# Performance work log

Measured on AMD Instinct MI355X. Metric: run time of the kernel, lower is better.

Reference implementation:

```python
import jax, jax.numpy as jnp
import numpy as np

H, W, N = 1024, 2048, 1572864
NF, NP, NIN = 32, 3, 5


def _linear_init(key, fan_in, fan_out):
    kw, kb = jax.random.split(key)
    bound = 1.0 / np.sqrt(fan_in)
    w = jax.random.uniform(kw, (fan_in, fan_out), jnp.float32, -bound, bound)
    b = jax.random.uniform(kb, (fan_out,), jnp.float32, -bound, bound)
    return w, b


def setup_inputs() -> dict:
    key = jax.random.key(0)
    ks = jax.random.split(key, 8)
    # grid: sub-pixel source coordinates, (2, N), x-row then y-row
    gx = jax.random.uniform(ks[0], (1, N), jnp.float32) * (W - 1)
    gy = jax.random.uniform(ks[1], (1, N), jnp.float32) * (H - 1)
    grid = jnp.concatenate([gx, gy], axis=0)
    # yi: unique flat pixel indices (torch index-assign assumes no duplicates)
    yi = jax.random.permutation(ks[2], H * W)[:N].astype(jnp.int32)
    # m: near-identity homography so the projective denominator stays well-conditioned
    m = jnp.eye(3, dtype=jnp.float32) + 0.05 * jax.random.normal(ks[3], (3, 3), jnp.float32)
    W1, b1 = _linear_init(ks[4], NIN, NF)
    W2, b2 = _linear_init(ks[5], NF, NF)
    W3, b3 = _linear_init(ks[6], NF, NF)
    W4, b4 = _linear_init(ks[7], NF, NP)
    return {"grid": grid, "yi": yi, "m": m,
            "W1": W1, "b1": b1, "W2": W2, "b2": b2,
            "W3": W3, "b3": b3, "W4": W4, "b4": b4,
            "size_h": H, "size_w": W}


def _calc_dsda_projective(m, h, w):
    # Area scale (Jacobian determinant magnitude) of the homography m at each
    # output pixel: |det(m)| / |m20*x + m21*y + m22|^3, flattened row-major (H*W,)
    xs = jnp.arange(w, dtype=jnp.float32)
    ys = jnp.arange(h, dtype=jnp.float32)
    denom = m[2, 0] * xs[None, :] + m[2, 1] * ys[:, None] + m[2, 2]  # (H, W)
    det = jnp.linalg.det(m)
    return (jnp.abs(det) / (jnp.abs(denom) ** 3)).reshape(-1)


def reference(grid, yi, m, W1, b1, W2, b2, W3, b3, W4, b4, size_h, size_w):
    h, w = size_h, size_w
    # --- feature construction (torch.no_grad block) ---
    dsda = _calc_dsda_projective(m, h, w)[yi][:, None]          # (N, 1) gather
    g = grid.T                                                  # (N, 2)
    gf = jnp.floor(g)
    tl = g - gf                                                 # x-fx, y-fy
    br = 1.0 - tl                                               # fx+1-x, fy+1-y
    x = jax.lax.stop_gradient(jnp.concatenate([tl, br, dsda], axis=1))  # (N, 5)
    # --- tiny 4-layer MLP ---
    hdd = jax.nn.relu(x @ W1 + b1)
    hdd = jax.nn.relu(hdd @ W2 + b2)
    hdd = jax.nn.relu(hdd @ W3 + b3)
    logits = hdd @ W4 + b4                                      # (N, NP)
    wgt = jax.nn.softmax(logits, axis=1)
    # --- scatter back to spatial layout ---
    w_spatial = jnp.zeros((h * w, NP), dtype=wgt.dtype).at[yi].set(wgt)
    return w_spatial.reshape(1, 1, h, w, NP)
```

## Files before the change

kernel.cpp:

```cpp
#include <hip/hip_runtime.h>


#define W_IMG 2048
#define NF    32
#define PST   80
#define BUF   (64 * PST)

typedef __attribute__((ext_vector_type(8))) _Float16 f16x8;
typedef __attribute__((ext_vector_type(4))) _Float16 f16x4;
typedef __attribute__((ext_vector_type(4))) float    f32x4;

__global__ __launch_bounds__(256) void fill_zero(float* __restrict__ out, int n) {
    int n4 = n >> 2;
    float4* o4 = (float4*)out;
    int stride = gridDim.x * blockDim.x;
    for (int i = blockIdx.x * blockDim.x + threadIdx.x; i < n4; i += stride)
        o4[i] = make_float4(0.f, 0.f, 0.f, 0.f);
    int t = (n4 << 2) + (blockIdx.x * blockDim.x + threadIdx.x);
    if (t < n) out[t] = 0.f;
}

__global__ __launch_bounds__(256, 4) void msampler_mlp(
    const float* __restrict__ grid,
    const int*   __restrict__ yi,
    const float* __restrict__ m,
    const float* __restrict__ W1, const float* __restrict__ b1,
    const float* __restrict__ W2, const float* __restrict__ b2,
    const float* __restrict__ W3, const float* __restrict__ b3,
    const float* __restrict__ W4, const float* __restrict__ b4,
    float* __restrict__ out, int N)
{
    const int tid  = threadIdx.x;
    const int lane = tid & 63;
    const int wave = tid >> 6;
    const int lm   = lane & 15;
    const int lq   = lane >> 4;
    const int i    = blockIdx.x * 256 + tid;
    const int ic   = i < N ? i : N - 1;

    __shared__ __align__(16) char smem[4 * 2 * BUF];
    char* bufA = smem + wave * (2 * BUF);
    char* bufB = bufA + BUF;

    f16x8 a1[2], a2[2], a3[2];
    f32x4 cb1[2], cb2[2], cb3[2];
#pragma unroll
    for (int mh = 0; mh < 2; ++mh) {
        int outc = 16 * mh + lm;
#pragma unroll
        for (int j = 0; j < 8; ++j) {
            int k = lq * 8 + j;
            a1[mh][j] = (k < 5) ? (_Float16)W1[k * NF + outc] : (_Float16)0.0f;
            a2[mh][j] = (_Float16)W2[k * NF + outc];
            a3[mh][j] = (_Float16)W3[k * NF + outc];
        }
#pragma unroll
        for (int r = 0; r < 4; ++r) {
            int o = 16 * mh + lq * 4 + r;
            cb1[mh][r] = b1[o];
            cb2[mh][r] = b2[o];
            cb3[mh][r] = b3[o];
        }
    }

    float gx = grid[ic];
    float gy = grid[N + ic];
    int   y  = yi[ic];
    int   py = y >> 11;
    int   px = y & (W_IMG - 1);

    float m00=m[0], m01=m[1], m02=m[2];
    float m10=m[3], m11=m[4], m12=m[5];
    float m20=m[6], m21=m[7], m22=m[8];
    float det = m00*(m11*m22 - m12*m21)
              - m01*(m10*m22 - m12*m20)
              + m02*(m10*m21 - m11*m20);
    float denom = m20*(float)px + m21*(float)py + m22;
    float ad    = fabsf(denom);
    float dsda  = fabsf(det) / (ad*ad*ad);
    dsda = fminf(dsda, 60000.f);

    float fx = gx - floorf(gx);
    float fy = gy - floorf(gy);

    {
        f16x8 f0;
        f0[0] = (_Float16)fx;        f0[1] = (_Float16)fy;
        f0[2] = (_Float16)(1.f-fx);  f0[3] = (_Float16)(1.f-fy);
        f0[4] = (_Float16)dsda;      f0[5] = (_Float16)0.0f;
        f0[6] = (_Float16)0.0f;      f0[7] = (_Float16)0.0f;
        f16x8 z = f0 - f0;
        char* row = bufA + lane * PST;
        *(f16x8*)(row)      = f0;
        *(f16x8*)(row + 16) = z;
        *(f16x8*)(row + 32) = z;
        *(f16x8*)(row + 48) = z;
    }
    __syncthreads();

#define MFMA_LAYER(SRC, DST, AF, CB)                                          \
    {                                                                         \
        f16x8 bf[4];                                                          \
        _Pragma("unroll")                                                     \
        for (int g = 0; g < 4; ++g)                                           \
            bf[g] = *(const f16x8*)((SRC) + (16*g + lm) * PST + lq * 16);     \
        _Pragma("unroll")                                                     \
        for (int mh = 0; mh < 2; ++mh) {                                      \
            _Pragma("unroll")                                                 \
            for (int g = 0; g < 4; ++g) {                                     \
                f32x4 d = __builtin_amdgcn_mfma_f32_16x16x32_f16(             \
                    AF[mh], bf[g], CB[mh], 0, 0, 0);                          \
                f16x4 o;                                                      \
                _Pragma("unroll")                                             \
                for (int r = 0; r < 4; ++r)                                   \
                    o[r] = (_Float16)fminf(fmaxf(d[r], 0.f), 60000.f);        \
                *(f16x4*)((DST) + (16*g + lm) * PST + (16*mh + lq*4) * 2) = o;\
            }                                                                 \
        }                                                                     \
    }

    MFMA_LAYER(bufA, bufB, a1, cb1)
    __syncthreads();
    MFMA_LAYER(bufB, bufA, a2, cb2)
    __syncthreads();
    MFMA_LAYER(bufA, bufB, a3, cb3)
    __syncthreads();
#undef MFMA_LAYER

    float l0 = b4[0], l1 = b4[1], l2 = b4[2];
    {
        const char* row = bufB + lane * PST;
#pragma unroll
        for (int c = 0; c < 4; ++c) {
            f16x8 hv = *(const f16x8*)(row + c * 16);
#pragma unroll
            for (int j = 0; j < 8; ++j) {
                float h = (float)hv[j];
                int k = c * 8 + j;
                l0 = fmaf(h, W4[k*3 + 0], l0);
                l1 = fmaf(h, W4[k*3 + 1], l1);
                l2 = fmaf(h, W4[k*3 + 2], l2);
            }
        }
    }
    float mx = fmaxf(l0, fmaxf(l1, l2));
    float e0 = __expf(l0 - mx), e1 = __expf(l1 - mx), e2 = __expf(l2 - mx);
    float inv = 1.f / (e0 + e1 + e2);

    if (i < N) {
        int o = y * 3;
        out[o + 0] = e0 * inv;
        out[o + 1] = e1 * inv;
        out[o + 2] = e2 * inv;
    }
}

extern "C" void kernel_launch(void* const* d_in, const int* in_sizes, int n_in,
                              void* d_out, int out_size, void* d_ws, size_t ws_size,
                              hipStream_t stream) {
    const float* grid = (const float*)d_in[0];
    const int*   yi   = (const int*)  d_in[1];
    const float* m    = (const float*)d_in[2];
    const float* W1   = (const float*)d_in[3];
    const float* b1   = (const float*)d_in[4];
    const float* W2   = (const float*)d_in[5];
    const float* b2   = (const float*)d_in[6];
    const float* W3   = (const float*)d_in[7];
    const float* b3   = (const float*)d_in[8];
    const float* W4   = (const float*)d_in[9];
    const float* b4   = (const float*)d_in[10];
    float* out = (float*)d_out;

    int N = in_sizes[1];

    fill_zero<<<1024, 256, 0, stream>>>(out, out_size);

    int block = 256;
    int grid_sz = (N + block - 1) / block;
    msampler_mlp<<<grid_sz, block, 0, stream>>>(
        grid, yi, m, W1, b1, W2, b2, W3, b3, W4, b4, out, N);
}
```

Before: 130.5 us.

## Process two tiles per wave with in-place MFMA buffer and MFMA final layer

```diff
diff --git a/kernel.cpp b/kernel.cpp
--- a/kernel.cpp
+++ b/kernel.cpp
@@ -3,8 +3,6 @@
 
 #define W_IMG 2048
 #define NF    32
-#define PST   80
-#define BUF   (64 * PST)
 
 typedef __attribute__((ext_vector_type(8))) _Float16 f16x8;
 typedef __attribute__((ext_vector_type(4))) _Float16 f16x4;
@@ -35,15 +33,12 @@
     const int wave = tid >> 6;
     const int lm   = lane & 15;
     const int lq   = lane >> 4;
-    const int i    = blockIdx.x * 256 + tid;
-    const int ic   = i < N ? i : N - 1;
-
-    __shared__ __align__(16) char smem[4 * 2 * BUF];
-    char* bufA = smem + wave * (2 * BUF);
-    char* bufB = bufA + BUF;
-
-    f16x8 a1[2], a2[2], a3[2];
-    f32x4 cb1[2], cb2[2], cb3[2];
+
+    __shared__ __align__(16) char smem[4 * 8192];
+    char* buf = smem + wave * 8192;
+
+    f16x8 a1[2], a2[2], a3[2], a4;
+    f32x4 cb1[2], cb2[2], cb3[2], cb4;
 #pragma unroll
     for (int mh = 0; mh < 2; ++mh) {
         int outc = 16 * mh + lm;
@@ -62,12 +57,16 @@
             cb3[mh][r] = b3[o];
         }
     }
-
-    float gx = grid[ic];
-    float gy = grid[N + ic];
-    int   y  = yi[ic];
-    int   py = y >> 11;
-    int   px = y & (W_IMG - 1);
+#pragma unroll
+    for (int j = 0; j < 8; ++j) {
+        int k = lq * 8 + j;
+        a4[j] = (lm < 3) ? (_Float16)W4[k * 3 + lm] : (_Float16)0.0f;
+    }
+#pragma unroll
+    for (int r = 0; r < 4; ++r) {
+        int o = lq * 4 + r;
+        cb4[r] = (o < 3) ? b4[o] : 0.f;
+    }
 
     float m00=m[0], m01=m[1], m02=m[2];
     float m10=m[3], m11=m[4], m12=m[5];
@@ -75,83 +74,103 @@
     float det = m00*(m11*m22 - m12*m21)
               - m01*(m10*m22 - m12*m20)
               + m02*(m10*m21 - m11*m20);
-    float denom = m20*(float)px + m21*(float)py + m22;
-    float ad    = fabsf(denom);
-    float dsda  = fabsf(det) / (ad*ad*ad);
-    dsda = fminf(dsda, 60000.f);
-
-    float fx = gx - floorf(gx);
-    float fy = gy - floorf(gy);
-
+    float adet = fabsf(det);
+
+    const int i0 = blockIdx.x * 512 + wave * 128;
+    int ya[2];
+#pragma unroll
+    for (int t = 0; t < 2; ++t) {
+        int i  = i0 + t * 64 + lane;
+        int ic = i < N ? i : N - 1;
+        float gx = grid[ic];
+        float gy = grid[N + ic];
+        int   y  = yi[ic];
+        ya[t] = y;
+        int py = y >> 11;
+        int px = y & (W_IMG - 1);
+        float denom = m20*(float)px + m21*(float)py + m22;
+        float ad    = fabsf(denom);
+        float dsda  = fminf(adet / (ad*ad*ad), 60000.f);
+        float fx = gx - floorf(gx);
+        float fy = gy - floorf(gy);
+        f16x8 f;
+        f[0] = (_Float16)fx;         f[1] = (_Float16)fy;
+        f[2] = (_Float16)(1.f-fx);   f[3] = (_Float16)(1.f-fy);
+        f[4] = (_Float16)dsda;       f[5] = (_Float16)0.0f;
+        f[6] = (_Float16)0.0f;       f[7] = (_Float16)0.0f;
+        int g = t * 4 + lq;
+        *(f16x8*)(buf + g * 1024 + lm * 16) = f;
+    }
     {
-        f16x8 f0;
-        f0[0] = (_Float16)fx;        f0[1] = (_Float16)fy;
-        f0[2] = (_Float16)(1.f-fx);  f0[3] = (_Float16)(1.f-fy);
-        f0[4] = (_Float16)dsda;      f0[5] = (_Float16)0.0f;
-        f0[6] = (_Float16)0.0f;      f0[7] = (_Float16)0.0f;
-        f16x8 z = f0 - f0;
-        char* row = bufA + lane * PST;
-        *(f16x8*)(row)      = f0;
-        *(f16x8*)(row + 16) = z;
-        *(f16x8*)(row + 32) = z;
-        *(f16x8*)(row + 48) = z;
-    }
-    __syncthreads();
-
-#define MFMA_LAYER(SRC, DST, AF, CB)                                          \
-    {                                                                         \
-        f16x8 bf[4];                                                          \
-        _Pragma("unroll")                                                     \
-        for (int g = 0; g < 4; ++g)                                           \
-            bf[g] = *(const f16x8*)((SRC) + (16*g + lm) * PST + lq * 16);     \
-        _Pragma("unroll")                                                     \
-        for (int mh = 0; mh < 2; ++mh) {                                      \
-            _Pragma("unroll")                                                 \
-            for (int g = 0; g < 4; ++g) {                                     \
-                f32x4 d = __builtin_amdgcn_mfma_f32_16x16x32_f16(             \
-                    AF[mh], bf[g], CB[mh], 0, 0, 0);                          \
-                f16x4 o;                                                      \
-                _Pragma("unroll")                                             \
-                for (int r = 0; r < 4; ++r)                                   \
-                    o[r] = (_Float16)fminf(fmaxf(d[r], 0.f), 60000.f);        \
-                *(f16x4*)((DST) + (16*g + lm) * PST + (16*mh + lq*4) * 2) = o;\
-            }                                                                 \
-        }                                                                     \
-    }
-
-    MFMA_LAYER(bufA, bufB, a1, cb1)
-    __syncthreads();
-    MFMA_LAYER(bufB, bufA, a2, cb2)
-    __syncthreads();
-    MFMA_LAYER(bufA, bufB, a3, cb3)
-    __syncthreads();
-#undef MFMA_LAYER
-
-    float l0 = b4[0], l1 = b4[1], l2 = b4[2];
-    {
-        const char* row = bufB + lane * PST;
-#pragma unroll
-        for (int c = 0; c < 4; ++c) {
-            f16x8 hv = *(const f16x8*)(row + c * 16);
-#pragma unroll
-            for (int j = 0; j < 8; ++j) {
-                float h = (float)hv[j];
-                int k = c * 8 + j;
-                l0 = fmaf(h, W4[k*3 + 0], l0);
-                l1 = fmaf(h, W4[k*3 + 1], l1);
-                l2 = fmaf(h, W4[k*3 + 2], l2);
-            }
-        }
-    }
-    float mx = fmaxf(l0, fmaxf(l1, l2));
-    float e0 = __expf(l0 - mx), e1 = __expf(l1 - mx), e2 = __expf(l2 - mx);
-    float inv = 1.f / (e0 + e1 + e2);
-
-    if (i < N) {
-        int o = y * 3;
-        out[o + 0] = e0 * inv;
-        out[o + 1] = e1 * inv;
-        out[o + 2] = e2 * inv;
+        f16x8 z = {};
+#pragma unroll
+        for (int j = 0; j < 6; ++j) {
+            int T  = lane >> 3;
+            int ch = (lane & 7) + 8 * j;
+            *(f16x8*)(buf + T * 1024 + 256 + ch * 16) = z;
+        }
+    }
+
+    const int woff = ((lq >> 1) * 16 + lm) * 16 + (lq & 1) * 8;
+
+#define LAYER(AF, CB)                                                          \
+    _Pragma("unroll")                                                          \
+    for (int tg = 0; tg < 2; ++tg) {                                           \
+        f16x8 bf[4];                                                           \
+        _Pragma("unroll")                                                      \
+        for (int q = 0; q < 4; ++q)                                            \
+            bf[q] = *(const f16x8*)(buf + (tg*4 + q) * 1024 + lane * 16);      \
+        _Pragma("unroll")                                                      \
+        for (int q = 0; q < 4; ++q) {                                          \
+            int T = tg * 4 + q;                                                \
+            _Pragma("unroll")                                                  \
+            for (int mh = 0; mh < 2; ++mh) {                                   \
+                f32x4 d = __builtin_amdgcn_mfma_f32_16x16x32_f16(              \
+                    AF[mh], bf[q], CB[mh], 0, 0, 0);                           \
+                f16x4 o;                                                       \
+                _Pragma("unroll")                                              \
+                for (int r = 0; r < 4; ++r)                                    \
+                    o[r] = (_Float16)fminf(fmaxf(d[r], 0.f), 60000.f);         \
+                *(f16x4*)(buf + T * 1024 + mh * 512 + woff) = o;               \
+            }                                                                  \
+        }                                                                      \
+    }
+
+    LAYER(a1, cb1)
+    LAYER(a2, cb2)
+    LAYER(a3, cb3)
+#undef LAYER
+
+#pragma unroll
+    for (int tg = 0; tg < 2; ++tg) {
+        f16x8 bf[4];
+#pragma unroll
+        for (int q = 0; q < 4; ++q)
+            bf[q] = *(const f16x8*)(buf + (tg*4 + q) * 1024 + lane * 16);
+#pragma unroll
+        for (int q = 0; q < 4; ++q) {
+            int T = tg * 4 + q;
+            f32x4 d = __builtin_amdgcn_mfma_f32_16x16x32_f16(a4, bf[q], cb4, 0, 0, 0);
+            if (lq == 0)
+                *(f32x4*)(buf + (T * 16 + lm) * 16) = d;
+        }
+    }
+
+#pragma unroll
+    for (int t = 0; t < 2; ++t) {
+        int s = t * 64 + lane;
+        f32x4 L = *(const f32x4*)(buf + s * 16);
+        float l0 = L[0], l1 = L[1], l2 = L[2];
+        float mx = fmaxf(l0, fmaxf(l1, l2));
+        float e0 = __expf(l0 - mx), e1 = __expf(l1 - mx), e2 = __expf(l2 - mx);
+        float inv = 1.f / (e0 + e1 + e2);
+        int i = i0 + s;
+        if (i < N) {
+            int o = ya[t] * 3;
+            out[o + 0] = e0 * inv;
+            out[o + 1] = e1 * inv;
+            out[o + 2] = e2 * inv;
+        }
     }
 }
 
@@ -175,8 +194,7 @@
 
     fill_zero<<<1024, 256, 0, stream>>>(out, out_size);
 
-    int block = 256;
-    int grid_sz = (N + block - 1) / block;
-    msampler_mlp<<<grid_sz, block, 0, stream>>>(
+    int grid_sz = (N + 511) / 512;
+    msampler_mlp<<<grid_sz, 256, 0, stream>>>(
         grid, yi, m, W1, b1, W2, b2, W3, b3, W4, b4, out, N);
 }
```

After: 129.5 us. About the same (-0.8%).
